# Kernel optimization log

Measured on AMD Instinct MI355X. Metric: run time of the kernel, lower is better.

Reference implementation:

```python
import jax, jax.numpy as jnp
import numpy as np

N_NODES = 4096
N_EDGES = 131072  # avg degree 32
N_STEPS = 1000


def setup_inputs() -> dict:
    key = jax.random.key(0)
    k1, k2, k3 = jax.random.split(key, 3)
    # Transition matrices: positive entries so the evidence division is well-conditioned.
    Qt = jax.random.uniform(k1, (N_STEPS, 2, 2), minval=0.1, maxval=1.0, dtype=jnp.float32)
    edge_index_x_t = jax.random.randint(k2, (2, N_EDGES), 0, N_NODES)
    edge_index_x_start = jax.random.randint(k3, (2, N_EDGES), 0, N_NODES)
    return {
        "Qt": Qt,
        "edge_index_x_t": edge_index_x_t,
        "edge_index_x_start": edge_index_x_start,
        "t": 500,
        "num_nodes": N_NODES,
    }


def _edge_index_to_adj(edge_index, num_nodes):
    # Dense binary adjacency, matching torch edge_index_to_adj.
    adj = jnp.zeros((num_nodes, num_nodes), dtype=jnp.int32)
    return adj.at[edge_index[0], edge_index[1]].set(1)


def reference(Qt, edge_index_x_t, edge_index_x_start, t, num_nodes):
    # q(x_{t-1} | x_t, x_0) = (Q0[:, x_t] * Q_{t-1}[x_0, :]) / Q_t[x_0, x_t]
    Q_likelihood = Qt[0]        # (2, 2)
    Q_prior = Qt[t - 1]         # (2, 2)  (batch of 1 identical time)
    Q_evidence = Qt[t]          # (2, 2)

    adj_x_t = _edge_index_to_adj(edge_index_x_t, num_nodes)      # (N, N) in {0,1}
    adj_x_start = _edge_index_to_adj(edge_index_x_start, num_nodes)

    # likelihood[i,j,k] = Q_likelihood[k, adj_x_t[i,j]]
    likelihood = jnp.transpose(Q_likelihood[:, adj_x_t], (1, 2, 0))  # (N, N, 2)
    # prior[i,j,:] = Q_prior[adj_x_start[i,j], :]
    prior = Q_prior[adj_x_start]                                     # (N, N, 2)
    # evidence[i,j] = Q_evidence[adj_x_start[i,j], adj_x_t[i,j]]
    evidence = Q_evidence[adj_x_start, adj_x_t][..., None]           # (N, N, 1)

    q_backward = likelihood * prior / evidence                       # (N, N, 2)

    # block_diag of a single triu(N,N,diag=1) mask == upper triangle (all possible edges)
    iu, ju = jnp.triu_indices(num_nodes, k=1)
    # forward returns q_backward_all[:, 1]
    return q_backward[iu, ju, 1]                                     # (N*(N-1)/2,)
```

## Files before the change

kernel.cpp:

```cpp
#include <hip/hip_runtime.h>
#include <cstdint>

#define N_NODES 4096
#define N_EDGES 131072
#define MASK_WORDS (N_NODES * N_NODES / 32)

__global__ void zero_ws_kernel(uint4* __restrict__ ws) {
    int idx = blockIdx.x * blockDim.x + threadIdx.x;
    ws[idx] = make_uint4(0u, 0u, 0u, 0u);
}

__global__ void scatter_edges_kernel(const int* __restrict__ et,
                                     const int* __restrict__ es,
                                     uint32_t* __restrict__ mask_t,
                                     uint32_t* __restrict__ mask_s) {
    int e = blockIdx.x * blockDim.x + threadIdx.x;
    if (e >= N_EDGES) return;
    {
        uint32_t i = (uint32_t)et[e];
        uint32_t j = (uint32_t)et[N_EDGES + e];
        uint32_t pos = i * N_NODES + j;
        atomicOr(&mask_t[pos >> 5], 1u << (pos & 31));
    }
    {
        uint32_t i = (uint32_t)es[e];
        uint32_t j = (uint32_t)es[N_EDGES + e];
        uint32_t pos = i * N_NODES + j;
        atomicOr(&mask_s[pos >> 5], 1u << (pos & 31));
    }
}

__global__ void fill_kernel(const float* __restrict__ Qt,
                            const int* __restrict__ t_ptr,
                            const uint32_t* __restrict__ mask_t,
                            const uint32_t* __restrict__ mask_s,
                            float* __restrict__ out) {
    const int t = t_ptr[0];
    const float l0 = Qt[2], l1 = Qt[3];
    const float p0 = Qt[(t - 1) * 4 + 1], p1 = Qt[(t - 1) * 4 + 3];
    const float e00 = Qt[t * 4 + 0], e01 = Qt[t * 4 + 1];
    const float e10 = Qt[t * 4 + 2], e11 = Qt[t * 4 + 3];
    float vals[4];
    vals[0] = l0 * p0 / e00;
    vals[1] = l1 * p0 / e01;
    vals[2] = l0 * p1 / e10;
    vals[3] = l1 * p1 / e11;

    const int i = blockIdx.x;
    const int base = i * (2 * N_NODES - i - 1) / 2;
    const uint32_t rowbits = (uint32_t)i * N_NODES;

    for (int j = i + 1 + threadIdx.x; j < N_NODES; j += blockDim.x) {
        uint32_t pos = rowbits + (uint32_t)j;
        uint32_t bt = (mask_t[pos >> 5] >> (pos & 31)) & 1u;
        uint32_t bs = (mask_s[pos >> 5] >> (pos & 31)) & 1u;
        out[base + (j - i - 1)] = vals[(bs << 1) | bt];
    }
}

extern "C" void kernel_launch(void* const* d_in, const int* in_sizes, int n_in,
                              void* d_out, int out_size, void* d_ws, size_t ws_size,
                              hipStream_t stream) {
    const float* Qt = (const float*)d_in[0];
    const int* et = (const int*)d_in[1];
    const int* es = (const int*)d_in[2];
    const int* t_ptr = (const int*)d_in[3];
    float* out = (float*)d_out;

    uint32_t* mask_t = (uint32_t*)d_ws;
    uint32_t* mask_s = mask_t + MASK_WORDS;

    zero_ws_kernel<<<(2 * MASK_WORDS / 4) / 256, 256, 0, stream>>>((uint4*)d_ws);
    scatter_edges_kernel<<<N_EDGES / 256, 256, 0, stream>>>(et, es, mask_t, mask_s);
    fill_kernel<<<N_NODES - 1, 256, 0, stream>>>(Qt, t_ptr, mask_t, mask_s, out);
}
```

Before: 92.16 us.

## Replace dense bitmasks with default fill plus sparse edge scatters into output

Drops the two dense adjacency bitmasks, along with their zeroing and atomic scatter. The kernel instead fills the whole triangular output with the no-edge value using float4 stores. It then scatters edge values directly into the output, first for x_t edges and then for x_start edges. The LSB of each stored float tags whether an x_t edge is present, so the second scatter can choose the right value without a separate mask. This removes the mask memory traffic and the per-element bit lookups, at the cost of perturbing output values by up to one ulp and doing uncoalesced scattered writes and reads.

```diff
diff --git a/kernel.cpp b/kernel.cpp
--- a/kernel.cpp
+++ b/kernel.cpp
@@ -3,58 +3,69 @@
 
 #define N_NODES 4096
 #define N_EDGES 131072
-#define MASK_WORDS (N_NODES * N_NODES / 32)
+#define OUT_QUADS (N_NODES * (N_NODES - 1) / 2 / 4)
 
-__global__ void zero_ws_kernel(uint4* __restrict__ ws) {
-    int idx = blockIdx.x * blockDim.x + threadIdx.x;
-    ws[idx] = make_uint4(0u, 0u, 0u, 0u);
-}
-
-__global__ void scatter_edges_kernel(const int* __restrict__ et,
-                                     const int* __restrict__ es,
-                                     uint32_t* __restrict__ mask_t,
-                                     uint32_t* __restrict__ mask_s) {
-    int e = blockIdx.x * blockDim.x + threadIdx.x;
-    if (e >= N_EDGES) return;
-    {
-        uint32_t i = (uint32_t)et[e];
-        uint32_t j = (uint32_t)et[N_EDGES + e];
-        uint32_t pos = i * N_NODES + j;
-        atomicOr(&mask_t[pos >> 5], 1u << (pos & 31));
-    }
-    {
-        uint32_t i = (uint32_t)es[e];
-        uint32_t j = (uint32_t)es[N_EDGES + e];
-        uint32_t pos = i * N_NODES + j;
-        atomicOr(&mask_s[pos >> 5], 1u << (pos & 31));
-    }
-}
-
-__global__ void fill_kernel(const float* __restrict__ Qt,
-                            const int* __restrict__ t_ptr,
-                            const uint32_t* __restrict__ mask_t,
-                            const uint32_t* __restrict__ mask_s,
-                            float* __restrict__ out) {
+__device__ __forceinline__ void compute_vals(const float* __restrict__ Qt,
+                                             const int* __restrict__ t_ptr,
+                                             float* vals) {
     const int t = t_ptr[0];
     const float l0 = Qt[2], l1 = Qt[3];
     const float p0 = Qt[(t - 1) * 4 + 1], p1 = Qt[(t - 1) * 4 + 3];
     const float e00 = Qt[t * 4 + 0], e01 = Qt[t * 4 + 1];
     const float e10 = Qt[t * 4 + 2], e11 = Qt[t * 4 + 3];
+    float v0 = l0 * p0 / e00;
+    float v1 = l1 * p0 / e01;
+    float v2 = l0 * p1 / e10;
+    float v3 = l1 * p1 / e11;
+    uint32_t u0 = __float_as_uint(v0) & ~1u;
+    uint32_t u1 = __float_as_uint(v1) |  1u;
+    uint32_t u2 = __float_as_uint(v2) & ~1u;
+    uint32_t u3 = __float_as_uint(v3) |  1u;
+    vals[0] = __uint_as_float(u0);
+    vals[1] = __uint_as_float(u1);
+    vals[2] = __uint_as_float(u2);
+    vals[3] = __uint_as_float(u3);
+}
+
+__device__ __forceinline__ int tri_idx(int i, int j) {
+    return i * (2 * N_NODES - i - 1) / 2 + (j - i - 1);
+}
+
+__global__ void gt_fill_default(const float* __restrict__ Qt,
+                                const int* __restrict__ t_ptr,
+                                float4* __restrict__ out) {
     float vals[4];
-    vals[0] = l0 * p0 / e00;
-    vals[1] = l1 * p0 / e01;
-    vals[2] = l0 * p1 / e10;
-    vals[3] = l1 * p1 / e11;
+    compute_vals(Qt, t_ptr, vals);
+    const float4 v = make_float4(vals[0], vals[0], vals[0], vals[0]);
+    int idx = blockIdx.x * blockDim.x + threadIdx.x;
+    out[idx] = v;
+}
 
-    const int i = blockIdx.x;
-    const int base = i * (2 * N_NODES - i - 1) / 2;
-    const uint32_t rowbits = (uint32_t)i * N_NODES;
+__global__ void gt_scatter_t(const float* __restrict__ Qt,
+                             const int* __restrict__ t_ptr,
+                             const int* __restrict__ et,
+                             float* __restrict__ out) {
+    float vals[4];
+    compute_vals(Qt, t_ptr, vals);
+    int e = blockIdx.x * blockDim.x + threadIdx.x;
+    int i = et[e];
+    int j = et[N_EDGES + e];
+    if (i < j) out[tri_idx(i, j)] = vals[1];
+}
 
-    for (int j = i + 1 + threadIdx.x; j < N_NODES; j += blockDim.x) {
-        uint32_t pos = rowbits + (uint32_t)j;
-        uint32_t bt = (mask_t[pos >> 5] >> (pos & 31)) & 1u;
-        uint32_t bs = (mask_s[pos >> 5] >> (pos & 31)) & 1u;
-        out[base + (j - i - 1)] = vals[(bs << 1) | bt];
+__global__ void gt_scatter_s(const float* __restrict__ Qt,
+                             const int* __restrict__ t_ptr,
+                             const int* __restrict__ es,
+                             float* __restrict__ out) {
+    float vals[4];
+    compute_vals(Qt, t_ptr, vals);
+    int e = blockIdx.x * blockDim.x + threadIdx.x;
+    int i = es[e];
+    int j = es[N_EDGES + e];
+    if (i < j) {
+        int idx = tri_idx(i, j);
+        uint32_t cur = __float_as_uint(out[idx]);
+        out[idx] = (cur & 1u) ? vals[3] : vals[2];
     }
 }
 
@@ -67,10 +78,7 @@
     const int* t_ptr = (const int*)d_in[3];
     float* out = (float*)d_out;
 
-    uint32_t* mask_t = (uint32_t*)d_ws;
-    uint32_t* mask_s = mask_t + MASK_WORDS;
-
-    zero_ws_kernel<<<(2 * MASK_WORDS / 4) / 256, 256, 0, stream>>>((uint4*)d_ws);
-    scatter_edges_kernel<<<N_EDGES / 256, 256, 0, stream>>>(et, es, mask_t, mask_s);
-    fill_kernel<<<N_NODES - 1, 256, 0, stream>>>(Qt, t_ptr, mask_t, mask_s, out);
+    gt_fill_default<<<OUT_QUADS / 256, 256, 0, stream>>>(Qt, t_ptr, (float4*)out);
+    gt_scatter_t<<<N_EDGES / 256, 256, 0, stream>>>(Qt, t_ptr, et, out);
+    gt_scatter_s<<<N_EDGES / 256, 256, 0, stream>>>(Qt, t_ptr, es, out);
 }
```

Measured after the change: 81.62 us. 1.13x faster.
